# Kernel tuning notes

Measured on AMD Instinct MI355X. Metric: run time of the kernel, lower is better.

## Reference

```python
import jax, jax.numpy as jnp
import numpy as np

N_NODES = 50000   # n_nodes (adjacency is [N,N])
NNZ = 800000      # nonzeros per support (avg degree 16)
S = 3             # number of supports
D_IN = 512
D_OUT = 256


def setup_inputs() -> dict:
    key = jax.random.key(0)
    k0, k1, k2, k3, k4, k5 = jax.random.split(key, 6)
    x = jax.random.normal(k0, (N_NODES, D_IN), dtype=jnp.float32)
    # glorot-uniform per-support weights, stacked [S, D_IN, D_OUT]
    scale = float(np.sqrt(6.0 / (D_IN + D_OUT)))
    W = jax.random.uniform(k1, (S, D_IN, D_OUT), dtype=jnp.float32, minval=-scale, maxval=scale)
    rows = jax.random.randint(k2, (S, NNZ), 0, N_NODES, dtype=jnp.int32)
    cols = jax.random.randint(k3, (S, NNZ), 0, N_NODES, dtype=jnp.int32)
    vals = jax.random.uniform(k4, (S, NNZ), dtype=jnp.float32)
    # Conv1d(in=S, out=1, k=1, bias=False) == learned weighted sum over supports
    cw = jax.random.normal(k5, (S,), dtype=jnp.float32) * 0.5
    return {"x": x, "W": W, "rows": rows, "cols": cols, "vals": vals, "cw": cw}


def reference(x, W, rows, cols, vals, cw):
    # mod='output': out = relu( sum_i cw[i] * (A_i @ (x @ W_i)) )
    def spmm(r, c, v, pre):
        # A in COO: out[r] += v * pre[c]
        msgs = v[:, None] * pre[c]          # [NNZ, D_OUT] gather
        return jax.ops.segment_sum(msgs, r, num_segments=N_NODES)

    out = jnp.zeros((N_NODES, D_OUT), dtype=x.dtype)
    for i in range(S):                      # small fixed support count
        pre = x @ W[i]                      # dense GEMM [N, D_OUT]
        out = out + cw[i] * spmm(rows[i], cols[i], vals[i], pre)
    return jax.nn.relu(out)
```

## Files before the change

kernel.cpp:

```cpp
#include <hip/hip_runtime.h>
#include <stdint.h>

#define N_NODES 50000
#define NNZ     800000
#define SUP     3
#define D_IN    512
#define D_OUT   256
#define TOT_E   (SUP * NNZ)
#define NBUCK   391
#define CAP     6976
#define CHUNK   6144

typedef __attribute__((ext_vector_type(8))) short bf16x8;
typedef __attribute__((ext_vector_type(4))) float f32x4;

static __device__ __forceinline__ unsigned short f2bf(float f) {
    unsigned int u = __float_as_uint(f);
    unsigned int r = (u + 0x7fffu + ((u >> 16) & 1u)) >> 16;
    return (unsigned short)r;
}
static __device__ __forceinline__ unsigned int pack_bf2(float lo, float hi) {
    unsigned int a = __float_as_uint(lo) + 0x8000u;
    unsigned int b = __float_as_uint(hi) + 0x8000u;
    return (a >> 16) | (b & 0xffff0000u);
}
static __device__ __forceinline__ float bf2f(unsigned short h) {
    return __uint_as_float(((unsigned int)h) << 16);
}

__global__ void wprep_kernel(const float* __restrict__ W, unsigned short* __restrict__ Wt) {
    int idx = blockIdx.x * 256 + threadIdx.x;
    if (idx >= SUP * D_IN * D_OUT) return;
    int n = idx & (D_OUT - 1);
    int k = (idx >> 8) & (D_IN - 1);
    int s = idx >> 17;
    Wt[((size_t)s * D_OUT + n) * D_IN + k] = f2bf(W[idx]);
}

__global__ __launch_bounds__(256) void bucket_kernel(const int* __restrict__ rows,
                                                     const int* __restrict__ cols,
                                                     const float* __restrict__ vals,
                                                     const float* __restrict__ cw,
                                                     int* __restrict__ bucket_cursor,
                                                     int2* __restrict__ buck) {
    __shared__ int hist[NBUCK];
    __shared__ int sc[256];
    __shared__ int sstart[NBUCK];
    __shared__ int lcur[NBUCK];
    __shared__ int gbase[NBUCK];
    __shared__ unsigned short bucket_of[CHUNK];
    __shared__ int2 stage[CHUNK];

    const int tid = threadIdx.x;
    const int base_n = blockIdx.x * CHUNK;
    const int count = min(CHUNK, TOT_E - base_n);
    float cw0 = cw[0], cw1 = cw[1], cw2 = cw[2];

    for (int i = tid; i < NBUCK; i += 256) hist[i] = 0;
    __syncthreads();
    for (int i = tid; i < count; i += 256) {
        atomicAdd(&hist[rows[base_n + i] >> 7], 1);
    }
    __syncthreads();
    int b0 = 2 * tid, b1 = b0 + 1;
    int h0 = (b0 < NBUCK) ? hist[b0] : 0;
    int h1 = (b1 < NBUCK) ? hist[b1] : 0;
    sc[tid] = h0 + h1;
    __syncthreads();
    for (int off = 1; off < 256; off <<= 1) {
        int t = (tid >= off) ? sc[tid - off] : 0;
        __syncthreads();
        sc[tid] += t;
        __syncthreads();
    }
    int excl = sc[tid] - (h0 + h1);
    if (b0 < NBUCK) { sstart[b0] = excl;      lcur[b0] = excl; }
    if (b1 < NBUCK) { sstart[b1] = excl + h0; lcur[b1] = excl + h0; }
    for (int i = tid; i < NBUCK; i += 256)
        gbase[i] = atomicAdd(&bucket_cursor[i], hist[i]);
    __syncthreads();
    for (int i = tid; i < count; i += 256) {
        int n = base_n + i;
        int r = rows[n];
        int c = cols[n];
        float v = vals[n];
        int s = n / NNZ;
        float w = v * (s == 0 ? cw0 : (s == 1 ? cw1 : cw2));
        int b = r >> 7;
        int p = atomicAdd(&lcur[b], 1);
        stage[p] = make_int2(((r & 127) << 18) | (s * N_NODES + c), __float_as_int(w));
        bucket_of[p] = (unsigned short)b;
    }
    __syncthreads();
    for (int i = tid; i < count; i += 256) {
        int b = bucket_of[i];
        int local_off = i - sstart[b];
        buck[(size_t)b * CAP + gbase[b] + local_off] = stage[i];
    }
}

__global__ __launch_bounds__(256) void sort_kernel(const int2* __restrict__ buck,
                                                   const int* __restrict__ bucket_cursor,
                                                   int2* __restrict__ cv,
                                                   int* __restrict__ base,
                                                   int* __restrict__ cnt) {
    __shared__ int hist[128];
    __shared__ int sc[128];
    __shared__ int sstart[128];
    __shared__ int cur[128];
    __shared__ int2 stage[CAP];

    const int b = blockIdx.x;
    const int tid = threadIdx.x;
    const int sz = bucket_cursor[b];
    const int2* src = buck + (size_t)b * CAP;

    if (tid < 128) hist[tid] = 0;
    __syncthreads();
    for (int i = tid; i < sz; i += 256) {
        atomicAdd(&hist[((unsigned)src[i].x) >> 18], 1);
    }
    __syncthreads();
    if (tid < 128) sc[tid] = hist[tid];
    __syncthreads();
    for (int off = 1; off < 128; off <<= 1) {
        int t = (tid >= off && tid < 128) ? sc[tid - off] : 0;
        __syncthreads();
        if (tid < 128) sc[tid] += t;
        __syncthreads();
    }
    if (tid < 128) {
        int st = sc[tid] - hist[tid];
        sstart[tid] = st;
        cur[tid] = st;
    }
    __syncthreads();
    for (int i = tid; i < sz; i += 256) {
        int2 e = src[i];
        int rl = ((unsigned)e.x) >> 18;
        int p = atomicAdd(&cur[rl], 1);
        stage[p] = make_int2(e.x & 0x3FFFF, e.y);
    }
    __syncthreads();
    size_t gb = (size_t)b * CAP;
    for (int i = tid; i < sz; i += 256) cv[gb + i] = stage[i];
    int r = b * 128 + tid;
    if (tid < 128 && r < N_NODES) {
        base[r] = (int)gb + sstart[tid];
        cnt[r]  = hist[tid];
    }
}

__global__ __launch_bounds__(256) void gemm_kernel(const float* __restrict__ x,
                                                   const unsigned short* __restrict__ Wt,
                                                   unsigned short* __restrict__ pre) {
    __shared__ unsigned short lds_a[128 * 40];
    __shared__ unsigned short lds_b[128 * 40];
    const int m0 = blockIdx.y * 128;
    const int n0 = (blockIdx.x & 1) * 128;
    const int s  = blockIdx.x >> 1;
    const unsigned short* wt = Wt + (size_t)s * D_OUT * D_IN;
    const int tid  = threadIdx.x;
    const int wave = tid >> 6;
    const int lane = tid & 63;
    const int quad = lane >> 4;
    const int lo   = lane & 15;
    const int wm = (wave & 1) * 64;
    const int wn = (wave >> 1) * 64;

    f32x4 acc[4][4] = {};

    const int ar = tid >> 1;
    const int ac = (tid & 1) * 16;
    const int gm = m0 + ar;
    const float* xrow = x + (size_t)gm * D_IN;
    const unsigned short* wrow = wt + (size_t)(n0 + ar) * D_IN;

    for (int kb = 0; kb < D_IN; kb += 32) {
        unsigned int aw[8];
        if (gm < N_NODES) {
            float4 f0 = *(const float4*)(xrow + kb + ac);
            float4 f1 = *(const float4*)(xrow + kb + ac + 4);
            float4 f2 = *(const float4*)(xrow + kb + ac + 8);
            float4 f3 = *(const float4*)(xrow + kb + ac + 12);
            aw[0] = pack_bf2(f0.x, f0.y); aw[1] = pack_bf2(f0.z, f0.w);
            aw[2] = pack_bf2(f1.x, f1.y); aw[3] = pack_bf2(f1.z, f1.w);
            aw[4] = pack_bf2(f2.x, f2.y); aw[5] = pack_bf2(f2.z, f2.w);
            aw[6] = pack_bf2(f3.x, f3.y); aw[7] = pack_bf2(f3.z, f3.w);
        } else {
            #pragma unroll
            for (int q = 0; q < 8; ++q) aw[q] = 0;
        }
        uint4 b0 = *(const uint4*)(wrow + kb + ac);
        uint4 b1 = *(const uint4*)(wrow + kb + ac + 8);

        __syncthreads();
        *(uint4*)&lds_a[ar * 40 + ac]     = make_uint4(aw[0], aw[1], aw[2], aw[3]);
        *(uint4*)&lds_a[ar * 40 + ac + 8] = make_uint4(aw[4], aw[5], aw[6], aw[7]);
        *(uint4*)&lds_b[ar * 40 + ac]     = b0;
        *(uint4*)&lds_b[ar * 40 + ac + 8] = b1;
        __syncthreads();

        bf16x8 af[4], bfr[4];
        #pragma unroll
        for (int i = 0; i < 4; ++i)
            af[i] = *(const bf16x8*)&lds_a[(wm + 16 * i + lo) * 40 + quad * 8];
        #pragma unroll
        for (int j = 0; j < 4; ++j)
            bfr[j] = *(const bf16x8*)&lds_b[(wn + 16 * j + lo) * 40 + quad * 8];
        #pragma unroll
        for (int i = 0; i < 4; ++i)
            #pragma unroll
            for (int j = 0; j < 4; ++j)
                acc[i][j] = __builtin_amdgcn_mfma_f32_16x16x32_bf16(af[i], bfr[j], acc[i][j], 0, 0, 0);
    }

    #pragma unroll
    for (int i = 0; i < 4; ++i) {
        #pragma unroll
        for (int j = 0; j < 4; ++j) {
            int gn = n0 + wn + 16 * j + lo;
            #pragma unroll
            for (int r = 0; r < 4; ++r) {
                int gm2 = m0 + wm + 16 * i + quad * 4 + r;
                if (gm2 < N_NODES)
                    pre[((size_t)s * N_NODES + gm2) * D_OUT + gn] = f2bf(acc[i][j][r]);
            }
        }
    }
}

__global__ __launch_bounds__(256) void spmm_kernel(const unsigned short* __restrict__ pre,
                                                   const int* __restrict__ base,
                                                   const int* __restrict__ cnt,
                                                   const int2* __restrict__ cv,
                                                   float* __restrict__ out) {
    int row  = blockIdx.x * 4 + (threadIdx.x >> 6);
    int lane = threadIdx.x & 63;
    int start = base[row];
    int end   = start + cnt[row];
    float a0 = 0.f, a1 = 0.f, a2 = 0.f, a3 = 0.f;
    int j = start;
    for (; j + 8 <= end; j += 8) {
        int2 e[8];
        #pragma unroll
        for (int q = 0; q < 8; ++q) e[q] = cv[j + q];
        ushort4 p[8];
        #pragma unroll
        for (int q = 0; q < 8; ++q)
            p[q] = *(const ushort4*)(pre + (size_t)e[q].x * D_OUT + lane * 4);
        #pragma unroll
        for (int q = 0; q < 8; ++q) {
            float w = __int_as_float(e[q].y);
            a0 += w * bf2f(p[q].x);
            a1 += w * bf2f(p[q].y);
            a2 += w * bf2f(p[q].z);
            a3 += w * bf2f(p[q].w);
        }
    }
    for (; j + 4 <= end; j += 4) {
        int2 e[4];
        #pragma unroll
        for (int q = 0; q < 4; ++q) e[q] = cv[j + q];
        ushort4 p[4];
        #pragma unroll
        for (int q = 0; q < 4; ++q)
            p[q] = *(const ushort4*)(pre + (size_t)e[q].x * D_OUT + lane * 4);
        #pragma unroll
        for (int q = 0; q < 4; ++q) {
            float w = __int_as_float(e[q].y);
            a0 += w * bf2f(p[q].x);
            a1 += w * bf2f(p[q].y);
            a2 += w * bf2f(p[q].z);
            a3 += w * bf2f(p[q].w);
        }
    }
    for (; j < end; ++j) {
        int2 e = cv[j];
        float w = __int_as_float(e.y);
        ushort4 p = *(const ushort4*)(pre + (size_t)e.x * D_OUT + lane * 4);
        a0 += w * bf2f(p.x);
        a1 += w * bf2f(p.y);
        a2 += w * bf2f(p.z);
        a3 += w * bf2f(p.w);
    }
    float4 o = make_float4(fmaxf(a0, 0.f), fmaxf(a1, 0.f), fmaxf(a2, 0.f), fmaxf(a3, 0.f));
    *(float4*)(out + (size_t)row * D_OUT + lane * 4) = o;
}

extern "C" void kernel_launch(void* const* d_in, const int* in_sizes, int n_in,
                              void* d_out, int out_size, void* d_ws, size_t ws_size,
                              hipStream_t stream) {
    const float* x    = (const float*)d_in[0];
    const float* W    = (const float*)d_in[1];
    const int*   rows = (const int*)d_in[2];
    const int*   cols = (const int*)d_in[3];
    const float* vals = (const float*)d_in[4];
    const float* cw   = (const float*)d_in[5];
    float* out = (float*)d_out;

    char* ws = (char*)d_ws;
    size_t off = 0;
    auto alloc = [&](size_t bytes) -> void* {
        void* p = ws + off;
        off += (bytes + 255) & ~(size_t)255;
        return p;
    };
    unsigned short* pre  = (unsigned short*)alloc((size_t)SUP * N_NODES * D_OUT * 2);
    unsigned short* Wt   = (unsigned short*)alloc((size_t)SUP * D_OUT * D_IN * 2);
    int* base            = (int*)alloc((size_t)N_NODES * 4);
    int* cnt             = (int*)alloc((size_t)N_NODES * 4);
    int* bucket_cursor   = (int*)alloc((size_t)NBUCK * 4);
    int2* cv             = (int2*)alloc((size_t)NBUCK * CAP * 8);
    int2* buck           = (int2*)pre;

    hipMemsetAsync(bucket_cursor, 0, (size_t)NBUCK * 4, stream);

    bucket_kernel<<<(TOT_E + CHUNK - 1) / CHUNK, 256, 0, stream>>>(rows, cols, vals, cw,
                                                                   bucket_cursor, buck);
    sort_kernel<<<NBUCK, 256, 0, stream>>>(buck, bucket_cursor, cv, base, cnt);
    wprep_kernel<<<(SUP * D_IN * D_OUT + 255) / 256, 256, 0, stream>>>(W, Wt);
    gemm_kernel<<<dim3(6, 391), 256, 0, stream>>>(x, Wt, pre);
    spmm_kernel<<<N_NODES / 4, 256, 0, stream>>>(pre, base, cnt, cv, out);
}
```

Baseline: 517.2 us.

## Pre-convert x to bf16 and stream GEMM tiles via direct global-to-LDS loads

Adds an xprep kernel that converts x to bf16 once, into a buffer padded to a multiple of 128 rows. Previously every GEMM block re-read fp32 x and converted it, and each row tile was redone by six blocks (3 supports × 2 column halves). The GEMM now fetches A and B tiles with global_load_lds (16-byte direct-to-LDS transfers), bypassing registers, and uses a K step of 64. The cost is an extra pass that writes and re-reads bf16 x. The new LDS layout also drops the row padding, which may cause bank conflicts on the fragment reads. Padding rows of xb are uninitialized, but their results are masked on store.

```diff
diff --git a/kernel.cpp b/kernel.cpp
--- a/kernel.cpp
+++ b/kernel.cpp
@@ -2,6 +2,7 @@
 #include <stdint.h>
 
 #define N_NODES 50000
+#define N_PAD   50048
 #define NNZ     800000
 #define SUP     3
 #define D_IN    512
@@ -13,6 +14,8 @@
 
 typedef __attribute__((ext_vector_type(8))) short bf16x8;
 typedef __attribute__((ext_vector_type(4))) float f32x4;
+typedef __attribute__((address_space(3))) unsigned int lds_u32_t;
+typedef const __attribute__((address_space(1))) unsigned int glb_u32_t;
 
 static __device__ __forceinline__ unsigned short f2bf(float f) {
     unsigned int u = __float_as_uint(f);
@@ -26,6 +29,20 @@
 }
 static __device__ __forceinline__ float bf2f(unsigned short h) {
     return __uint_as_float(((unsigned int)h) << 16);
+}
+
+__global__ void xprep_kernel(const float* __restrict__ x, unsigned int* __restrict__ xb) {
+    int idx = blockIdx.x * 256 + threadIdx.x;
+    if (idx >= N_NODES * D_IN / 8) return;
+    const float4* src = (const float4*)(x) + idx * 2;
+    float4 f0 = src[0];
+    float4 f1 = src[1];
+    uint4 o;
+    o.x = pack_bf2(f0.x, f0.y);
+    o.y = pack_bf2(f0.z, f0.w);
+    o.z = pack_bf2(f1.x, f1.y);
+    o.w = pack_bf2(f1.z, f1.w);
+    *((uint4*)xb + idx) = o;
 }
 
 __global__ void wprep_kernel(const float* __restrict__ W, unsigned short* __restrict__ Wt) {
@@ -151,11 +168,11 @@
     }
 }
 
-__global__ __launch_bounds__(256) void gemm_kernel(const float* __restrict__ x,
+__global__ __launch_bounds__(256) void gemm_kernel(const unsigned short* __restrict__ xb,
                                                    const unsigned short* __restrict__ Wt,
                                                    unsigned short* __restrict__ pre) {
-    __shared__ unsigned short lds_a[128 * 40];
-    __shared__ unsigned short lds_b[128 * 40];
+    __shared__ unsigned short lds_a[128 * 64];
+    __shared__ unsigned short lds_b[128 * 64];
     const int m0 = blockIdx.y * 128;
     const int n0 = (blockIdx.x & 1) * 128;
     const int s  = blockIdx.x >> 1;
@@ -170,49 +187,37 @@
 
     f32x4 acc[4][4] = {};
 
-    const int ar = tid >> 1;
-    const int ac = (tid & 1) * 16;
-    const int gm = m0 + ar;
-    const float* xrow = x + (size_t)gm * D_IN;
-    const unsigned short* wrow = wt + (size_t)(n0 + ar) * D_IN;
-
-    for (int kb = 0; kb < D_IN; kb += 32) {
-        unsigned int aw[8];
-        if (gm < N_NODES) {
-            float4 f0 = *(const float4*)(xrow + kb + ac);
-            float4 f1 = *(const float4*)(xrow + kb + ac + 4);
-            float4 f2 = *(const float4*)(xrow + kb + ac + 8);
-            float4 f3 = *(const float4*)(xrow + kb + ac + 12);
-            aw[0] = pack_bf2(f0.x, f0.y); aw[1] = pack_bf2(f0.z, f0.w);
-            aw[2] = pack_bf2(f1.x, f1.y); aw[3] = pack_bf2(f1.z, f1.w);
-            aw[4] = pack_bf2(f2.x, f2.y); aw[5] = pack_bf2(f2.z, f2.w);
-            aw[6] = pack_bf2(f3.x, f3.y); aw[7] = pack_bf2(f3.z, f3.w);
-        } else {
+    for (int kb = 0; kb < D_IN; kb += 64) {
+        __syncthreads();
+        #pragma unroll
+        for (int c = 0; c < 4; ++c) {
+            int idx = c * 256 + tid;
+            int row = idx >> 3;
+            int kp  = idx & 7;
+            const unsigned short* ga = xb + (size_t)(m0 + row) * D_IN + kb + kp * 8;
+            __builtin_amdgcn_global_load_lds((glb_u32_t*)ga,
+                                             (lds_u32_t*)&lds_a[idx * 8], 16, 0, 0);
+            const unsigned short* gb = wt + (size_t)(n0 + row) * D_IN + kb + kp * 8;
+            __builtin_amdgcn_global_load_lds((glb_u32_t*)gb,
+                                             (lds_u32_t*)&lds_b[idx * 8], 16, 0, 0);
+        }
+        __syncthreads();
+
+        #pragma unroll
+        for (int t = 0; t < 2; ++t) {
+            bf16x8 af[4], bfr[4];
             #pragma unroll
-            for (int q = 0; q < 8; ++q) aw[q] = 0;
-        }
-        uint4 b0 = *(const uint4*)(wrow + kb + ac);
-        uint4 b1 = *(const uint4*)(wrow + kb + ac + 8);
-
-        __syncthreads();
-        *(uint4*)&lds_a[ar * 40 + ac]     = make_uint4(aw[0], aw[1], aw[2], aw[3]);
-        *(uint4*)&lds_a[ar * 40 + ac + 8] = make_uint4(aw[4], aw[5], aw[6], aw[7]);
-        *(uint4*)&lds_b[ar * 40 + ac]     = b0;
-        *(uint4*)&lds_b[ar * 40 + ac + 8] = b1;
-        __syncthreads();
-
-        bf16x8 af[4], bfr[4];
-        #pragma unroll
-        for (int i = 0; i < 4; ++i)
-            af[i] = *(const bf16x8*)&lds_a[(wm + 16 * i + lo) * 40 + quad * 8];
-        #pragma unroll
-        for (int j = 0; j < 4; ++j)
-            bfr[j] = *(const bf16x8*)&lds_b[(wn + 16 * j + lo) * 40 + quad * 8];
-        #pragma unroll
-        for (int i = 0; i < 4; ++i)
+            for (int i = 0; i < 4; ++i)
+                af[i] = *(const bf16x8*)&lds_a[(wm + 16 * i + lo) * 64 + t * 32 + quad * 8];
             #pragma unroll
             for (int j = 0; j < 4; ++j)
-                acc[i][j] = __builtin_amdgcn_mfma_f32_16x16x32_bf16(af[i], bfr[j], acc[i][j], 0, 0, 0);
+                bfr[j] = *(const bf16x8*)&lds_b[(wn + 16 * j + lo) * 64 + t * 32 + quad * 8];
+            #pragma unroll
+            for (int i = 0; i < 4; ++i)
+                #pragma unroll
+                for (int j = 0; j < 4; ++j)
+                    acc[i][j] = __builtin_amdgcn_mfma_f32_16x16x32_bf16(af[i], bfr[j], acc[i][j], 0, 0, 0);
+        }
     }
 
     #pragma unroll
@@ -307,6 +312,7 @@
         return p;
     };
     unsigned short* pre  = (unsigned short*)alloc((size_t)SUP * N_NODES * D_OUT * 2);
+    unsigned short* xb   = (unsigned short*)alloc((size_t)N_PAD * D_IN * 2);
     unsigned short* Wt   = (unsigned short*)alloc((size_t)SUP * D_OUT * D_IN * 2);
     int* base            = (int*)alloc((size_t)N_NODES * 4);
     int* cnt             = (int*)alloc((size_t)N_NODES * 4);
@@ -319,7 +325,8 @@
     bucket_kernel<<<(TOT_E + CHUNK - 1) / CHUNK, 256, 0, stream>>>(rows, cols, vals, cw,
                                                                    bucket_cursor, buck);
     sort_kernel<<<NBUCK, 256, 0, stream>>>(buck, bucket_cursor, cv, base, cnt);
+    xprep_kernel<<<(N_NODES * D_IN / 8 + 255) / 256, 256, 0, stream>>>(x, (unsigned int*)xb);
     wprep_kernel<<<(SUP * D_IN * D_OUT + 255) / 256, 256, 0, stream>>>(W, Wt);
-    gemm_kernel<<<dim3(6, 391), 256, 0, stream>>>(x, Wt, pre);
+    gemm_kernel<<<dim3(6, 391), 256, 0, stream>>>(xb, Wt, pre);
     spmm_kernel<<<N_NODES / 4, 256, 0, stream>>>(pre, base, cnt, cv, out);
 }
```

Measured after the change: 493.0 us. 1.05x faster.
